# Optimization experiments

Measured on AMD Instinct MI355X. Metric: run time of the kernel, lower is better.

The kernel has to match this reference:

```python
import jax, jax.numpy as jnp
import numpy as np

NUM_TRUE = 8
NUM_NULL = 2
NUM_EXPERTS = NUM_TRUE + NUM_NULL
TOP_K = 2


def setup_inputs() -> dict:
    key = jax.random.key(0)
    k0, k1, k2 = jax.random.split(key, 3)
    B, S, D = 4, 2048, 1024
    inputs = jax.random.normal(k0, (B, S, D), dtype=jnp.float32)
    gate_w = jax.random.normal(k1, (NUM_EXPERTS, D), dtype=jnp.float32) * 0.02
    gate_b = jnp.zeros((NUM_EXPERTS,), dtype=jnp.float32)
    # expert_w stored as [E, D_in, D_out] so expert i computes x @ expert_w[i] + expert_b[i]
    expert_w = jax.random.normal(k2, (NUM_TRUE, D, D), dtype=jnp.float32) * 0.02
    expert_b = jnp.zeros((NUM_TRUE, D), dtype=jnp.float32)
    return {"inputs": inputs, "gate_w": gate_w, "gate_b": gate_b,
            "expert_w": expert_w, "expert_b": expert_b}


def reference(inputs, gate_w, gate_b, expert_w, expert_b):
    D = inputs.shape[-1]
    x = inputs.reshape(-1, D)                       # [T, D]
    gate_logits = x @ gate_w.T + gate_b             # [T, E]
    gate_probs = jax.nn.softmax(gate_logits, axis=-1)
    weights, selected = jax.lax.top_k(gate_probs, TOP_K)  # [T, K]
    true_mask = selected < NUM_TRUE                 # null experts contribute nothing
    true_weights = weights * true_mask
    denom = true_weights.sum(axis=-1, keepdims=True)
    denom = jnp.where(denom > 0, denom, jnp.ones_like(denom))
    norm_w = (true_weights / denom).astype(x.dtype)  # [T, K]
    # per-(token, true-expert) combine weight; zero for unselected experts
    one_hot = jax.nn.one_hot(selected, NUM_EXPERTS, dtype=norm_w.dtype)  # [T, K, E]
    combine_w = jnp.einsum('tk,tke->te', norm_w, one_hot)[:, :NUM_TRUE]  # [T, E_true]
    # dense expert evaluation, then weighted combine (zero weights cancel
    # exactly as the gather/scatter loop in the torch code)
    expert_out = jnp.einsum('td,edh->teh', x, expert_w) + expert_b[None, :, :]  # [T, E_true, D]
    out = jnp.einsum('te,teh->th', combine_w, expert_out)  # [T, D]
    return out.reshape(inputs.shape[:-1] + (out.shape[-1],))
```

## Files before the change

### kernel.cpp

```cpp
#include <hip/hip_runtime.h>
#include <hip/hip_bf16.h>
#include <stdint.h>

#define T_TOKENS 8192
#define D_DIM    1024
#define NE       10
#define NT       8
#define SEG      2048

typedef unsigned short u16;
typedef __attribute__((ext_vector_type(8))) __bf16 bf16x8;
typedef __attribute__((ext_vector_type(4))) float  f32x4;
typedef __attribute__((ext_vector_type(8))) unsigned short u16x8;
typedef __attribute__((ext_vector_type(4))) unsigned short u16x4;

static __device__ __forceinline__ u16 f32_to_bf16(float f) {
  union { float f; uint32_t u; } v; v.f = f;
  uint32_t u = v.u;
  return (u16)((u + 0x7fffu + ((u >> 16) & 1u)) >> 16);
}
static __device__ __forceinline__ float bf16_to_f32(u16 u) {
  union { uint32_t u; float f; } v; v.u = ((uint32_t)u) << 16; return v.f;
}

static __device__ __forceinline__ void async_load16(const u16* g, u16* l) {
  __builtin_amdgcn_global_load_lds(
      (const __attribute__((address_space(1))) void*)(const void*)g,
      (__attribute__((address_space(3))) void*)(void*)l, 16, 0, 0);
}


union PrepShared {
  struct { float gws[NE * D_DIM]; float gbs[NE]; int se[16]; float swt[16]; } g;
  struct { float tile[64][68]; } t;
};

__global__ __launch_bounds__(256) void prep_kernel(
    const float* __restrict__ x, const float* __restrict__ gw,
    const float* __restrict__ gb, const float* __restrict__ W,
    u16* __restrict__ xb, u16* __restrict__ wT,
    int* __restrict__ cnt, int* __restrict__ tokList,
    int* __restrict__ revIdx, float* __restrict__ revW) {
  __shared__ PrepShared sh;
  int tid = threadIdx.x;

  if (blockIdx.x >= 1024) {
    int tb = blockIdx.x - 1024;
    int e  = tb >> 8;
    int rem = tb & 255;
    int k0 = (rem >> 4) * 64;
    int n0 = (rem & 15) * 64;
    int cr = tid & 15;
    int r0 = tid >> 4;
    const float* We = W + ((size_t)e << 20);
#pragma unroll
    for (int pass = 0; pass < 4; ++pass) {
      int r = pass * 16 + r0;
      f32x4 v = *(const f32x4*)&We[(size_t)(k0 + r) * 1024 + n0 + cr * 4];
#pragma unroll
      for (int j = 0; j < 4; ++j) sh.t.tile[cr * 4 + j][r] = v[j];
    }
    __syncthreads();
    u16* wTe = wT + ((size_t)e << 20);
#pragma unroll
    for (int pass = 0; pass < 4; ++pass) {
      int n = pass * 16 + r0;
      f32x4 tv = *(const f32x4*)&sh.t.tile[n][cr * 4];
      u16x4 pk;
#pragma unroll
      for (int j = 0; j < 4; ++j) pk[j] = f32_to_bf16(tv[j]);
      *(u16x4*)&wTe[(size_t)(n0 + n) * 1024 + k0 + cr * 4] = pk;
    }
    return;
  }

  {
    const f32x4* g4 = (const f32x4*)gw;
    f32x4* s4 = (f32x4*)sh.g.gws;
    for (int i = tid; i < NE * D_DIM / 4; i += 256) s4[i] = g4[i];
  }
  if (tid < NE) sh.g.gbs[tid] = gb[tid];
  __syncthreads();
  int lane = tid & 63;
  int wv   = tid >> 6;
  const f32x4* gws4 = (const f32x4*)sh.g.gws;
  for (int it = 0; it < 2; ++it) {
    int slot = wv * 2 + it;
    int t = blockIdx.x * 8 + slot;
    const f32x4* xr4 = (const f32x4*)(x + (size_t)t * D_DIM);
    f32x4 xv[4];
#pragma unroll
    for (int jj = 0; jj < 4; ++jj) xv[jj] = xr4[lane + 64 * jj];
    u16x4* xbr = (u16x4*)(xb + (size_t)t * D_DIM);
#pragma unroll
    for (int jj = 0; jj < 4; ++jj) {
      u16x4 pk;
#pragma unroll
      for (int k = 0; k < 4; ++k) pk[k] = f32_to_bf16(xv[jj][k]);
      xbr[lane + 64 * jj] = pk;
    }
    float logit[NE];
#pragma unroll
    for (int e = 0; e < NE; ++e) {
      float a = 0.f;
#pragma unroll
      for (int jj = 0; jj < 4; ++jj) {
        f32x4 gv = gws4[e * 256 + lane + 64 * jj];
#pragma unroll
        for (int k = 0; k < 4; ++k) a = fmaf(xv[jj][k], gv[k], a);
      }
#pragma unroll
      for (int off = 32; off >= 1; off >>= 1) a += __shfl_xor(a, off);
      logit[e] = a + sh.g.gbs[e];
    }
    float mx = logit[0];
#pragma unroll
    for (int e = 1; e < NE; ++e) mx = fmaxf(mx, logit[e]);
    float p[NE]; float s = 0.f;
#pragma unroll
    for (int e = 0; e < NE; ++e) { p[e] = expf(logit[e] - mx); s += p[e]; }
    int e0 = 0; float b0 = p[0];
#pragma unroll
    for (int e = 1; e < NE; ++e) if (p[e] > b0) { b0 = p[e]; e0 = e; }
    int e1 = -1; float b1 = -1.f;
#pragma unroll
    for (int e = 0; e < NE; ++e) if (e != e0 && p[e] > b1) { b1 = p[e]; e1 = e; }
    float w0 = b0 / s, w1 = b1 / s;
    float tw0 = (e0 < NT) ? w0 : 0.f;
    float tw1 = (e1 < NT) ? w1 : 0.f;
    float denom = tw0 + tw1;
    float nw0 = 0.f, nw1 = 0.f;
    if (denom > 0.f) { nw0 = tw0 / denom; nw1 = tw1 / denom; }
    if (lane == 0) {
      sh.g.se[slot * 2]     = (e0 < NT) ? e0 : -1;  sh.g.swt[slot * 2]     = nw0;
      sh.g.se[slot * 2 + 1] = (e1 < NT) ? e1 : -1;  sh.g.swt[slot * 2 + 1] = nw1;
      if (e0 >= NT) { revIdx[t * 2]     = -1; revW[t * 2]     = 0.f; }
      if (e1 >= NT) { revIdx[t * 2 + 1] = -1; revW[t * 2 + 1] = 0.f; }
    }
  }
  __syncthreads();
  if (tid < NT) {
    int e = tid, c = 0;
    for (int i = 0; i < 16; ++i) c += (sh.g.se[i] == e);
    if (c > 0) {
      int base = atomicAdd(&cnt[e * 32], c);
      int j = 0;
      for (int i = 0; i < 16; ++i) {
        if (sh.g.se[i] == e) {
          int tt  = blockIdx.x * 8 + (i >> 1);
          int pos = base + j;
          tokList[e * SEG + pos]   = tt;
          revIdx[tt * 2 + (i & 1)] = e * SEG + pos;
          revW[tt * 2 + (i & 1)]   = sh.g.swt[i];
          ++j;
        }
      }
    }
  }
}

__global__ __launch_bounds__(512) void moe_gemm(
    const u16* __restrict__ xb, const u16* __restrict__ wT,
    const int* __restrict__ cnt, const int* __restrict__ tokList,
    const float* __restrict__ eb, u16* __restrict__ ybuf) {
  int e  = blockIdx.x;
  int c  = cnt[e * 32];
  int m0 = blockIdx.z * 256;
  if (m0 >= c) return;
  int n0 = blockIdx.y * 256;
  __shared__ __align__(16) u16 As[2][256 * 64];
  __shared__ __align__(16) u16 Bs[2][256 * 64];
  __shared__ int tokS[256];
  int tid = threadIdx.x;
  if (tid < 256) {
    int gm = m0 + tid;
    tokS[tid] = (gm < c) ? tokList[e * SEG + gm] : tokList[e * SEG];
  }
  __syncthreads();
  int lane = tid & 63;
  int wv   = tid >> 6;
  int sub = lane >> 3;
  int chd = (lane & 7) ^ sub;
  const u16* gA[4];
#pragma unroll
  for (int j = 0; j < 4; ++j) {
    int tok = tokS[wv * 32 + j * 8 + sub];
    gA[j] = xb + (size_t)tok * 1024 + chd * 8;
  }
  const u16* wTe = wT + ((size_t)e << 20);
  const u16* gB  = wTe + (size_t)(n0 + wv * 32 + sub) * 1024 + chd * 8;
  int ldsW = (wv * 32) * 64;

  int wm = wv >> 2, wn = wv & 3;
  int lrow = lane & 15;
  int q    = lane >> 4;
  int pk0 = ((q)     ^ (lrow & 7)) * 8;
  int pk1 = ((4 + q) ^ (lrow & 7)) * 8;
  f32x4 acc[8][4];
#pragma unroll
  for (int i = 0; i < 8; ++i)
#pragma unroll
    for (int j = 0; j < 4; ++j) acc[i][j] = (f32x4){0.f, 0.f, 0.f, 0.f};

#pragma unroll
  for (int j = 0; j < 4; ++j) {
    async_load16(gA[j], As[0] + ldsW + j * 512);
    async_load16(gB + j * 8192, Bs[0] + ldsW + j * 512);
  }

  int cur = 0;
  for (int kt = 0; kt < 16; ++kt) {
    asm volatile("s_barrier" ::: "memory");
    if (kt < 15) {
      int nx = cur ^ 1;
      int ko = (kt + 1) * 64;
#pragma unroll
      for (int j = 0; j < 4; ++j) {
        async_load16(gA[j] + ko, As[nx] + ldsW + j * 512);
        async_load16(gB + j * 8192 + ko, Bs[nx] + ldsW + j * 512);
      }
      asm volatile("s_waitcnt vmcnt(8)" ::: "memory");
    } else {
      asm volatile("s_waitcnt vmcnt(0)" ::: "memory");
    }
    asm volatile("s_barrier" ::: "memory");
    const u16* Ab = As[cur];
    const u16* Bb = Bs[cur];
    bf16x8 bfr[4], af[4];
#pragma unroll
    for (int nt = 0; nt < 4; ++nt)
      bfr[nt] = *(const bf16x8*)(Bb + (wn * 64 + nt * 16 + lrow) * 64 + pk0);
#pragma unroll
    for (int mt = 0; mt < 4; ++mt)
      af[mt] = *(const bf16x8*)(Ab + (wm * 128 + mt * 16 + lrow) * 64 + pk0);
    __builtin_amdgcn_s_setprio(1);
#pragma unroll
    for (int mt = 0; mt < 4; ++mt)
#pragma unroll
      for (int nt = 0; nt < 4; ++nt)
        acc[mt][nt] = __builtin_amdgcn_mfma_f32_16x16x32_bf16(
            af[mt], bfr[nt], acc[mt][nt], 0, 0, 0);
    __builtin_amdgcn_s_setprio(0);
    asm volatile("s_barrier" ::: "memory");
#pragma unroll
    for (int mt = 0; mt < 4; ++mt)
      af[mt] = *(const bf16x8*)(Ab + (wm * 128 + (mt + 4) * 16 + lrow) * 64 + pk0);
    __builtin_amdgcn_s_setprio(1);
#pragma unroll
    for (int mt = 0; mt < 4; ++mt)
#pragma unroll
      for (int nt = 0; nt < 4; ++nt)
        acc[mt + 4][nt] = __builtin_amdgcn_mfma_f32_16x16x32_bf16(
            af[mt], bfr[nt], acc[mt + 4][nt], 0, 0, 0);
    __builtin_amdgcn_s_setprio(0);
    asm volatile("s_barrier" ::: "memory");
#pragma unroll
    for (int nt = 0; nt < 4; ++nt)
      bfr[nt] = *(const bf16x8*)(Bb + (wn * 64 + nt * 16 + lrow) * 64 + pk1);
#pragma unroll
    for (int mt = 0; mt < 4; ++mt)
      af[mt] = *(const bf16x8*)(Ab + (wm * 128 + mt * 16 + lrow) * 64 + pk1);
    __builtin_amdgcn_s_setprio(1);
#pragma unroll
    for (int mt = 0; mt < 4; ++mt)
#pragma unroll
      for (int nt = 0; nt < 4; ++nt)
        acc[mt][nt] = __builtin_amdgcn_mfma_f32_16x16x32_bf16(
            af[mt], bfr[nt], acc[mt][nt], 0, 0, 0);
    __builtin_amdgcn_s_setprio(0);
    asm volatile("s_barrier" ::: "memory");
#pragma unroll
    for (int mt = 0; mt < 4; ++mt)
      af[mt] = *(const bf16x8*)(Ab + (wm * 128 + (mt + 4) * 16 + lrow) * 64 + pk1);
    __builtin_amdgcn_s_setprio(1);
#pragma unroll
    for (int mt = 0; mt < 4; ++mt)
#pragma unroll
      for (int nt = 0; nt < 4; ++nt)
        acc[mt + 4][nt] = __builtin_amdgcn_mfma_f32_16x16x32_bf16(
            af[mt], bfr[nt], acc[mt + 4][nt], 0, 0, 0);
    __builtin_amdgcn_s_setprio(0);
    cur ^= 1;
  }
  int rq = lane >> 4;
  float bias[4];
#pragma unroll
  for (int nt = 0; nt < 4; ++nt)
    bias[nt] = eb[e * 1024 + n0 + wn * 64 + nt * 16 + lrow];
  u16* yb = ybuf + ((size_t)(e * SEG + m0)) * 1024 + n0 + wn * 64 + lrow;
#pragma unroll
  for (int mt = 0; mt < 8; ++mt) {
#pragma unroll
    for (int r = 0; r < 4; ++r) {
      int ml = wm * 128 + mt * 16 + rq * 4 + r;
      u16* row = yb + (size_t)ml * 1024;
#pragma unroll
      for (int nt = 0; nt < 4; ++nt)
        row[nt * 16] = f32_to_bf16(acc[mt][nt][r] + bias[nt]);
    }
  }
}

__global__ __launch_bounds__(256) void combine_kernel(
    const u16* __restrict__ ybuf, const int* __restrict__ revIdx,
    const float* __restrict__ revW, float* __restrict__ out) {
  int tid = threadIdx.x, lane = tid & 63, wv = tid >> 6;
  int t  = blockIdx.x * 4 + wv;
  int i0 = revIdx[t * 2], i1 = revIdx[t * 2 + 1];
  float w0 = revW[t * 2], w1 = revW[t * 2 + 1];
  float o[16];
#pragma unroll
  for (int k = 0; k < 16; ++k) o[k] = 0.f;
  if (i0 >= 0) {
    const u16x8* y = (const u16x8*)(ybuf + (size_t)i0 * 1024);
#pragma unroll
    for (int jj = 0; jj < 2; ++jj) {
      u16x8 v = y[lane + 64 * jj];
#pragma unroll
      for (int k = 0; k < 8; ++k) o[jj * 8 + k] += w0 * bf16_to_f32(v[k]);
    }
  }
  if (i1 >= 0) {
    const u16x8* y = (const u16x8*)(ybuf + (size_t)i1 * 1024);
#pragma unroll
    for (int jj = 0; jj < 2; ++jj) {
      u16x8 v = y[lane + 64 * jj];
#pragma unroll
      for (int k = 0; k < 8; ++k) o[jj * 8 + k] += w1 * bf16_to_f32(v[k]);
    }
  }
  f32x4* o4 = (f32x4*)(out + (size_t)t * 1024);
#pragma unroll
  for (int jj = 0; jj < 2; ++jj)
#pragma unroll
    for (int h = 0; h < 2; ++h) {
      f32x4 vv = {o[jj * 8 + h * 4], o[jj * 8 + h * 4 + 1],
                  o[jj * 8 + h * 4 + 2], o[jj * 8 + h * 4 + 3]};
      __builtin_nontemporal_store(vv, &o4[2 * (lane + 64 * jj) + h]);
    }
}

extern "C" void kernel_launch(void* const* d_in, const int* in_sizes, int n_in,
                              void* d_out, int out_size, void* d_ws, size_t ws_size,
                              hipStream_t stream) {
  const float* x  = (const float*)d_in[0];
  const float* gw = (const float*)d_in[1];
  const float* gb = (const float*)d_in[2];
  const float* ew = (const float*)d_in[3];
  const float* eb = (const float*)d_in[4];
  float* out = (float*)d_out;
  char* ws = (char*)d_ws;
  int*   cnt     = (int*)ws;
  int*   tokList = (int*)(ws + 4096);
  int*   revIdx  = (int*)(ws + 4096 + 65536);
  float* revW    = (float*)(ws + 4096 + 131072);
  u16*   xb      = (u16*)(ws + 200704);
  u16*   wT      = (u16*)(ws + 200704 + 16777216);
  u16*   ybuf    = (u16*)(ws + 200704 + 33554432);

  hipMemsetAsync(cnt, 0, 4096, stream);
  prep_kernel<<<3072, 256, 0, stream>>>(x, gw, gb, ew, xb, wT, cnt, tokList,
                                        revIdx, revW);
  moe_gemm<<<dim3(8, 4, 8), 512, 0, stream>>>(xb, wT, cnt, tokList, eb, ybuf);
  combine_kernel<<<2048, 256, 0, stream>>>(ybuf, revIdx, revW, out);
}
```

Baseline: 178.9 us.

## Interleave next-tile global prefetch with MFMA phases in expert GEMM loop

Restructures the K-loop of the expert GEMM so the eight async global-to-LDS loads for the next tile are split into four pairs, each issued between an LDS fragment read and an MFMA phase, instead of all at once at the top of the loop. The wait moves to a full vmcnt(0) plus barrier at the end of each iteration, and separate registers hold the low and high A fragments. The aim is to spread memory issue across compute and avoid a burst of loads before the math starts. In exchange the loop now waits for all prefetches before the next iteration, which may expose load latency, and it adds register pressure.

```diff
diff --git a/kernel.cpp b/kernel.cpp
--- a/kernel.cpp
+++ b/kernel.cpp
@@ -207,51 +207,54 @@
     async_load16(gA[j], As[0] + ldsW + j * 512);
     async_load16(gB + j * 8192, Bs[0] + ldsW + j * 512);
   }
+  asm volatile("s_waitcnt vmcnt(0)" ::: "memory");
+  asm volatile("s_barrier" ::: "memory");
 
   int cur = 0;
   for (int kt = 0; kt < 16; ++kt) {
-    asm volatile("s_barrier" ::: "memory");
-    if (kt < 15) {
-      int nx = cur ^ 1;
-      int ko = (kt + 1) * 64;
-#pragma unroll
-      for (int j = 0; j < 4; ++j) {
-        async_load16(gA[j] + ko, As[nx] + ldsW + j * 512);
-        async_load16(gB + j * 8192 + ko, Bs[nx] + ldsW + j * 512);
-      }
-      asm volatile("s_waitcnt vmcnt(8)" ::: "memory");
-    } else {
-      asm volatile("s_waitcnt vmcnt(0)" ::: "memory");
-    }
-    asm volatile("s_barrier" ::: "memory");
     const u16* Ab = As[cur];
     const u16* Bb = Bs[cur];
-    bf16x8 bfr[4], af[4];
+    int nx = cur ^ 1;
+    int ko = (kt + 1) * 64;
+    int pf = (kt < 15);
+    bf16x8 bfr[4], afl[4], afh[4];
 #pragma unroll
     for (int nt = 0; nt < 4; ++nt)
       bfr[nt] = *(const bf16x8*)(Bb + (wn * 64 + nt * 16 + lrow) * 64 + pk0);
 #pragma unroll
     for (int mt = 0; mt < 4; ++mt)
-      af[mt] = *(const bf16x8*)(Ab + (wm * 128 + mt * 16 + lrow) * 64 + pk0);
+      afl[mt] = *(const bf16x8*)(Ab + (wm * 128 + mt * 16 + lrow) * 64 + pk0);
+    if (pf) {
+      async_load16(gA[0] + ko, As[nx] + ldsW);
+      async_load16(gA[1] + ko, As[nx] + ldsW + 512);
+    }
+    asm volatile("s_barrier" ::: "memory");
+    asm volatile("s_waitcnt lgkmcnt(0)" ::: "memory");
     __builtin_amdgcn_s_setprio(1);
 #pragma unroll
     for (int mt = 0; mt < 4; ++mt)
 #pragma unroll
       for (int nt = 0; nt < 4; ++nt)
         acc[mt][nt] = __builtin_amdgcn_mfma_f32_16x16x32_bf16(
-            af[mt], bfr[nt], acc[mt][nt], 0, 0, 0);
+            afl[mt], bfr[nt], acc[mt][nt], 0, 0, 0);
     __builtin_amdgcn_s_setprio(0);
     asm volatile("s_barrier" ::: "memory");
 #pragma unroll
     for (int mt = 0; mt < 4; ++mt)
-      af[mt] = *(const bf16x8*)(Ab + (wm * 128 + (mt + 4) * 16 + lrow) * 64 + pk0);
+      afh[mt] = *(const bf16x8*)(Ab + (wm * 128 + (mt + 4) * 16 + lrow) * 64 + pk0);
+    if (pf) {
+      async_load16(gA[2] + ko, As[nx] + ldsW + 1024);
+      async_load16(gA[3] + ko, As[nx] + ldsW + 1536);
+    }
+    asm volatile("s_barrier" ::: "memory");
+    asm volatile("s_waitcnt lgkmcnt(0)" ::: "memory");
     __builtin_amdgcn_s_setprio(1);
 #pragma unroll
     for (int mt = 0; mt < 4; ++mt)
 #pragma unroll
       for (int nt = 0; nt < 4; ++nt)
         acc[mt + 4][nt] = __builtin_amdgcn_mfma_f32_16x16x32_bf16(
-            af[mt], bfr[nt], acc[mt + 4][nt], 0, 0, 0);
+            afh[mt], bfr[nt], acc[mt + 4][nt], 0, 0, 0);
     __builtin_amdgcn_s_setprio(0);
     asm volatile("s_barrier" ::: "memory");
 #pragma unroll
@@ -259,27 +262,41 @@
       bfr[nt] = *(const bf16x8*)(Bb + (wn * 64 + nt * 16 + lrow) * 64 + pk1);
 #pragma unroll
     for (int mt = 0; mt < 4; ++mt)
-      af[mt] = *(const bf16x8*)(Ab + (wm * 128 + mt * 16 + lrow) * 64 + pk1);
+      afl[mt] = *(const bf16x8*)(Ab + (wm * 128 + mt * 16 + lrow) * 64 + pk1);
+    if (pf) {
+      async_load16(gB + ko, Bs[nx] + ldsW);
+      async_load16(gB + 8192 + ko, Bs[nx] + ldsW + 512);
+    }
+    asm volatile("s_barrier" ::: "memory");
+    asm volatile("s_waitcnt lgkmcnt(0)" ::: "memory");
     __builtin_amdgcn_s_setprio(1);
 #pragma unroll
     for (int mt = 0; mt < 4; ++mt)
 #pragma unroll
       for (int nt = 0; nt < 4; ++nt)
         acc[mt][nt] = __builtin_amdgcn_mfma_f32_16x16x32_bf16(
-            af[mt], bfr[nt], acc[mt][nt], 0, 0, 0);
+            afl[mt], bfr[nt], acc[mt][nt], 0, 0, 0);
     __builtin_amdgcn_s_setprio(0);
     asm volatile("s_barrier" ::: "memory");
 #pragma unroll
     for (int mt = 0; mt < 4; ++mt)
-      af[mt] = *(const bf16x8*)(Ab + (wm * 128 + (mt + 4) * 16 + lrow) * 64 + pk1);
+      afh[mt] = *(const bf16x8*)(Ab + (wm * 128 + (mt + 4) * 16 + lrow) * 64 + pk1);
+    if (pf) {
+      async_load16(gB + 16384 + ko, Bs[nx] + ldsW + 1024);
+      async_load16(gB + 24576 + ko, Bs[nx] + ldsW + 1536);
+    }
+    asm volatile("s_barrier" ::: "memory");
+    asm volatile("s_waitcnt lgkmcnt(0)" ::: "memory");
     __builtin_amdgcn_s_setprio(1);
 #pragma unroll
     for (int mt = 0; mt < 4; ++mt)
 #pragma unroll
       for (int nt = 0; nt < 4; ++nt)
         acc[mt + 4][nt] = __builtin_amdgcn_mfma_f32_16x16x32_bf16(
-            af[mt], bfr[nt], acc[mt + 4][nt], 0, 0, 0);
+            afh[mt], bfr[nt], acc[mt + 4][nt], 0, 0, 0);
     __builtin_amdgcn_s_setprio(0);
+    asm volatile("s_waitcnt vmcnt(0)" ::: "memory");
+    asm volatile("s_barrier" ::: "memory");
     cur ^= 1;
   }
   int rq = lane >> 4;
```

Measured after the change: 173.8 us. 2.9% less time.
